# Optimization experiments

Measured on AMD Instinct MI355X. Metric: run time of the kernel, lower is better.

## Reference

```python
import jax, jax.numpy as jnp
import numpy as np

DIM = 1024
HEADS = 16
DIM_HEAD = 64
INNER = HEADS * DIM_HEAD  # 1024
MLP = 4096
EPS = 1e-5


def layer_norm(x, gamma, beta):
    mu = jnp.mean(x, axis=-1, keepdims=True)
    var = jnp.var(x, axis=-1, keepdims=True)
    return (x - mu) * jax.lax.rsqrt(var + EPS) * gamma + beta


def setup_inputs() -> dict:
    key = jax.random.key(0)
    ks = jax.random.split(key, 10)
    s = 0.02
    return {
        "x": jax.random.normal(ks[0], (2, 2048, DIM), dtype=jnp.float32),
        "ln1_g": jnp.ones((DIM,), jnp.float32),
        "ln1_b": jnp.zeros((DIM,), jnp.float32),
        "w_qkv": jax.random.normal(ks[1], (DIM, 3 * INNER), jnp.float32) * s,
        "w_out": jax.random.normal(ks[2], (INNER, DIM), jnp.float32) * s,
        "b_out": jnp.zeros((DIM,), jnp.float32),
        "ln2_g": jnp.ones((DIM,), jnp.float32),
        "ln2_b": jnp.zeros((DIM,), jnp.float32),
        "w1": jax.random.normal(ks[3], (DIM, MLP), jnp.float32) * s,
        "b1": jnp.zeros((MLP,), jnp.float32),
        "w2": jax.random.normal(ks[4], (MLP, DIM), jnp.float32) * s,
        "b2": jnp.zeros((DIM,), jnp.float32),
    }


def reference(x, ln1_g, ln1_b, w_qkv, w_out, b_out, ln2_g, ln2_b, w1, b1, w2, b2):
    b, n, _ = x.shape
    scale = DIM_HEAD ** -0.5

    # --- attention sublayer (pre-norm) ---
    h = layer_norm(x, ln1_g, ln1_b)
    qkv = h @ w_qkv  # [b, n, 3*inner]
    q, k, v = jnp.split(qkv, 3, axis=-1)
    # [b, n, inner] -> [b, heads, n, dim_head]
    def to_heads(t):
        return t.reshape(b, n, HEADS, DIM_HEAD).transpose(0, 2, 1, 3)
    q, k, v = to_heads(q), to_heads(k), to_heads(v)
    dots = jnp.einsum('bhid,bhjd->bhij', q, k) * scale  # [b,h,n,n]
    attn = jax.nn.softmax(dots, axis=-1)
    out = jnp.einsum('bhij,bhjd->bhid', attn, v)
    out = out.transpose(0, 2, 1, 3).reshape(b, n, INNER)
    x = out @ w_out + b_out + x

    # --- FFN sublayer (pre-norm) ---
    h = layer_norm(x, ln2_g, ln2_b)
    h = jax.nn.gelu(h @ w1 + b1, approximate=False)
    x = h @ w2 + b2 + x
    return x
```

## Files before the change

### kernel.cpp

```cpp
#include <hip/hip_runtime.h>
#include <hip/hip_bf16.h>
#include <math.h>

#define SEQ 2048
#define BATCH 2
#define TOKENS 4096
#define HEADS 16
#define DHEAD 64
#define TOKSTRIDE 3072

typedef __attribute__((ext_vector_type(4))) float f32x4;
typedef __attribute__((ext_vector_type(16))) float f32x16;
typedef __attribute__((ext_vector_type(8))) __bf16 bf16x8;
typedef __attribute__((ext_vector_type(8))) unsigned short ushort8;
typedef __attribute__((ext_vector_type(4))) unsigned short ushort4_t;
typedef __attribute__((ext_vector_type(4))) unsigned u32x4;
typedef __attribute__((ext_vector_type(2))) unsigned u32x2;

#if __has_builtin(__builtin_amdgcn_exp2f)
#define EXP2(x) __builtin_amdgcn_exp2f(x)
#else
#define EXP2(x) exp2f(x)
#endif

#if __has_builtin(__builtin_amdgcn_permlane32_swap)
#define HAS_PL32 1
#else
#define HAS_PL32 0
#endif

__device__ __forceinline__ unsigned short f2bf(float f) {
  unsigned u = __builtin_bit_cast(unsigned, f);
  u += 0x7fffu + ((u >> 16) & 1u);
  return (unsigned short)(u >> 16);
}

__device__ __forceinline__ float bf2f(unsigned short s) {
  unsigned u = ((unsigned)s) << 16;
  return __builtin_bit_cast(float, u);
}

__device__ __forceinline__ unsigned cvt_pk_bf16(float lo, float hi) {
  unsigned r;
  asm("v_cvt_pk_bf16_f32 %0, %1, %2" : "=v"(r) : "v"(lo), "v"(hi));
  return r;
}

__device__ __forceinline__ void cp16(const void* g, void* l) {
  __builtin_amdgcn_global_load_lds((const __attribute__((address_space(1))) void*)g,
                                   (__attribute__((address_space(3))) void*)l, 16, 0, 0);
}

#define FENCE asm volatile("" ::: "memory")
#define BARR  do { FENCE; __builtin_amdgcn_s_barrier(); FENCE; } while (0)

__global__ __launch_bounds__(256) void ln_rows(const float* __restrict__ x,
                                               const float* __restrict__ g,
                                               const float* __restrict__ b,
                                               unsigned short* __restrict__ out) {
  const int row = blockIdx.x;
  const int t = threadIdx.x;
  const f32x4* x4 = (const f32x4*)(x + (size_t)row * 1024);
  f32x4 v = x4[t];
  float sum = v[0] + v[1] + v[2] + v[3];
  float ss  = v[0]*v[0] + v[1]*v[1] + v[2]*v[2] + v[3]*v[3];
#pragma unroll
  for (int off = 1; off < 64; off <<= 1) {
    sum += __shfl_xor(sum, off);
    ss  += __shfl_xor(ss, off);
  }
  __shared__ float red[8];
  const int w = t >> 6, l = t & 63;
  if (l == 0) { red[w] = sum; red[w + 4] = ss; }
  __syncthreads();
  sum = red[0] + red[1] + red[2] + red[3];
  ss  = red[4] + red[5] + red[6] + red[7];
  const float mean = sum * (1.0f / 1024.0f);
  const float var  = ss * (1.0f / 1024.0f) - mean * mean;
  const float rs = rsqrtf(var + 1e-5f);
  ushort4_t o;
#pragma unroll
  for (int j = 0; j < 4; ++j) {
    float gv = g[t * 4 + j], bv = b[t * 4 + j];
    o[j] = f2bf((v[j] - mean) * rs * gv + bv);
  }
  *(ushort4_t*)(out + (size_t)row * 1024 + t * 4) = o;
}

__global__ __launch_bounds__(256) void ln_rows_bf(const unsigned short* __restrict__ x,
                                                  const float* __restrict__ g,
                                                  const float* __restrict__ b,
                                                  unsigned short* __restrict__ out) {
  const int row = blockIdx.x;
  const int t = threadIdx.x;
  ushort4_t v4 = *(const ushort4_t*)(x + (size_t)row * 1024 + t * 4);
  float v[4] = {bf2f(v4[0]), bf2f(v4[1]), bf2f(v4[2]), bf2f(v4[3])};
  float sum = v[0] + v[1] + v[2] + v[3];
  float ss  = v[0]*v[0] + v[1]*v[1] + v[2]*v[2] + v[3]*v[3];
#pragma unroll
  for (int off = 1; off < 64; off <<= 1) {
    sum += __shfl_xor(sum, off);
    ss  += __shfl_xor(ss, off);
  }
  __shared__ float red[8];
  const int w = t >> 6, l = t & 63;
  if (l == 0) { red[w] = sum; red[w + 4] = ss; }
  __syncthreads();
  sum = red[0] + red[1] + red[2] + red[3];
  ss  = red[4] + red[5] + red[6] + red[7];
  const float mean = sum * (1.0f / 1024.0f);
  const float var  = ss * (1.0f / 1024.0f) - mean * mean;
  const float rs = rsqrtf(var + 1e-5f);
  ushort4_t o;
#pragma unroll
  for (int j = 0; j < 4; ++j) {
    float gv = g[t * 4 + j], bv = b[t * 4 + j];
    o[j] = f2bf((v[j] - mean) * rs * gv + bv);
  }
  *(ushort4_t*)(out + (size_t)row * 1024 + t * 4) = o;
}

__global__ __launch_bounds__(256) void transpose_cast(const float* __restrict__ w,
                                                      unsigned short* __restrict__ wt,
                                                      int K, int N, float scale, int nscaled) {
  __shared__ float tile[32][33];
  const int n0 = blockIdx.x * 32, k0 = blockIdx.y * 32;
  const int tx = threadIdx.x & 31;
  const int ty = threadIdx.x >> 5;
#pragma unroll
  for (int i = 0; i < 4; ++i)
    tile[ty + 8 * i][tx] = w[(size_t)(k0 + ty + 8 * i) * N + n0 + tx];
  __syncthreads();
#pragma unroll
  for (int i = 0; i < 4; ++i) {
    int n = n0 + ty + 8 * i;
    float s = (n < nscaled) ? scale : 1.0f;
    wt[(size_t)n * K + k0 + tx] = f2bf(tile[tx][ty + 8 * i] * s);
  }
}

template <int EPI, int BN, int MINW>
__global__ __launch_bounds__(256, MINW) void gemm_bt(
    const unsigned short* __restrict__ A, const unsigned short* __restrict__ Bt,
    void* __restrict__ Cp, const float* __restrict__ bias, const void* __restrict__ resv,
    int M, int N, int K) {
  constexpr int BM = 128, BK = 64;
  constexpr int MR = BM / 32, NR = BN / 32;
  constexpr int AIT = BM * BK / 2048;
  constexpr int BIT = BN * BK / 2048;
  __shared__ unsigned short la[BM * BK];
  __shared__ unsigned short lb[BN * BK];
  const int t = threadIdx.x;
  const int w = t >> 6, l = t & 63;
  const int nwg = gridDim.x;
  const int bid = blockIdx.x;
  const int bid2 = (bid & 7) * (nwg >> 3) + (bid >> 3);
  const int nx = N / BN;
  const int m0 = (bid2 / nx) * BM, n0 = (bid2 % nx) * BN;
  const int wr = w >> 1, wc = w & 1;
  const int lrow = l & 15, lk4 = l >> 4;
  f32x4 acc[MR][NR] = {};

  for (int k0 = 0; k0 < K; k0 += BK) {
#pragma unroll
    for (int i = 0; i < AIT; ++i) {
      int idx = t + 256 * i;
      int row = idx >> 3, seg = idx & 7;
      int ss = seg ^ (row & 7);
      cp16(A + (size_t)(m0 + row) * K + k0 + ss * 8, (char*)la + w * 1024 + i * 4096);
    }
#pragma unroll
    for (int i = 0; i < BIT; ++i) {
      int idx = t + 256 * i;
      int row = idx >> 3, seg = idx & 7;
      int ss = seg ^ (row & 7);
      cp16(Bt + (size_t)(n0 + row) * K + k0 + ss * 8, (char*)lb + w * 1024 + i * 4096);
    }
    __syncthreads();
#pragma unroll
    for (int ks = 0; ks < 2; ++ks) {
      bf16x8 af[MR], bfr[NR];
#pragma unroll
      for (int mi = 0; mi < MR; ++mi) {
        int row = wr * (BM / 2) + mi * 16 + lrow;
        int ss = (ks * 4 + lk4) ^ (row & 7);
        af[mi] = *(const bf16x8*)((const char*)la + row * 128 + ss * 16);
      }
#pragma unroll
      for (int ni = 0; ni < NR; ++ni) {
        int row = wc * (BN / 2) + ni * 16 + lrow;
        int ss = (ks * 4 + lk4) ^ (row & 7);
        bfr[ni] = *(const bf16x8*)((const char*)lb + row * 128 + ss * 16);
      }
#pragma unroll
      for (int mi = 0; mi < MR; ++mi)
#pragma unroll
        for (int ni = 0; ni < NR; ++ni)
          acc[mi][ni] = __builtin_amdgcn_mfma_f32_16x16x32_bf16(af[mi], bfr[ni], acc[mi][ni], 0, 0, 0);
    }
    __syncthreads();
  }

#pragma unroll
  for (int mi = 0; mi < MR; ++mi) {
    int rowb = m0 + wr * (BM / 2) + mi * 16 + lk4 * 4;
#pragma unroll
    for (int ni = 0; ni < NR; ++ni) {
      int col = n0 + wc * (BN / 2) + ni * 16 + lrow;
      f32x4 a = acc[mi][ni];
#pragma unroll
      for (int r = 0; r < 4; ++r) {
        size_t off = (size_t)(rowb + r) * N + col;
        if (EPI == 0) {
          ((unsigned short*)Cp)[off] = f2bf(a[r]);
        } else if (EPI == 2) {
          float v = a[r] + bias[col];
          ((unsigned short*)Cp)[off] = f2bf(0.5f * v * (1.0f + erff(v * 0.70710678f)));
        } else if (EPI == 3) {
          ((unsigned short*)Cp)[off] = f2bf(a[r] + bias[col] + ((const float*)resv)[off]);
        } else {
          ((float*)Cp)[off] = a[r] + bias[col] + bf2f(((const unsigned short*)resv)[off]);
        }
      }
    }
  }
}

__global__ __launch_bounds__(256, 2) void attn4(const unsigned short* __restrict__ qkv,
                                                unsigned short* __restrict__ Op,
                                                float2* __restrict__ ml) {
  __shared__ unsigned short lk_[64 * 64];
  __shared__ unsigned short lvt[64 * 64];
  const int t = threadIdx.x, wv = t >> 6, l = t & 63;
  const int chunk = blockIdx.x & 3, qb = blockIdx.x >> 2;
  const int h = blockIdx.y, b = blockIdx.z;
  const size_t tok0 = (size_t)b * SEQ;
  const int lq = l & 31, hi = l >> 5, l7 = l & 7;
  const int qrow = qb * 128 + wv * 32 + lq;
  const int kstart = chunk * 8;

  bf16x8 qf[4];
#pragma unroll
  for (int dc = 0; dc < 4; ++dc)
    qf[dc] = *(const bf16x8*)(qkv + (tok0 + qrow) * TOKSTRIDE + h * DHEAD + dc * 16 + hi * 8);

  float mrun = -1e30f, lsum = 0.0f;
  f32x16 o0 = {}, o1 = {};

  {
#pragma unroll
    for (int i = 0; i < 2; ++i) {
      int idx = t + 256 * i;
      int key = idx >> 3, seg = idx & 7;
      cp16(qkv + (tok0 + kstart * 64 + key) * TOKSTRIDE + 1024 + h * DHEAD + ((seg ^ (key & 7)) << 3),
           (char*)lk_ + wv * 1024 + i * 4096);
    }
#pragma unroll
    for (int i = 0; i < 2; ++i) {
      int idx = t + 256 * i;
      int key = idx & 63, seg = idx >> 6;
      ushort8 v8 = *(const ushort8*)(qkv + (tok0 + kstart * 64 + key) * TOKSTRIDE + 2048 + h * DHEAD + seg * 8);
#pragma unroll
      for (int j = 0; j < 8; ++j) {
        int d = seg * 8 + j;
        lvt[d * 64 + (((key >> 3) ^ (d & 7)) << 3) + (key & 7)] = v8[j];
      }
    }
  }
  __syncthreads();

  for (int kb = 0; kb < 8; ++kb) {
    const bool more = (kb + 1 < 8);
    const int kpre = kstart + kb + 1;

    f32x16 s0 = {}, s1 = {};
    __builtin_amdgcn_s_setprio(1);
#pragma unroll
    for (int dc = 0; dc < 4; ++dc) {
      int sgA = (dc * 2 + hi) ^ l7;
      bf16x8 kf0 = *(const bf16x8*)((const char*)lk_ + lq * 128 + (sgA << 4));
      bf16x8 kf1 = *(const bf16x8*)((const char*)lk_ + (32 + lq) * 128 + (sgA << 4));
      s0 = __builtin_amdgcn_mfma_f32_32x32x16_bf16(kf0, qf[dc], s0, 0, 0, 0);
      s1 = __builtin_amdgcn_mfma_f32_32x32x16_bf16(kf1, qf[dc], s1, 0, 0, 0);
    }
    __builtin_amdgcn_s_setprio(0);

    asm volatile("s_waitcnt lgkmcnt(0)" ::: "memory");
    BARR;
    __builtin_amdgcn_sched_barrier(0);

    ushort8 vpre[2];
    if (more) {
#pragma unroll
      for (int i = 0; i < 2; ++i) {
        int idx = t + 256 * i;
        int key = idx >> 3, seg = idx & 7;
        cp16(qkv + (tok0 + kpre * 64 + key) * TOKSTRIDE + 1024 + h * DHEAD + ((seg ^ (key & 7)) << 3),
             (char*)lk_ + wv * 1024 + i * 4096);
      }
#pragma unroll
      for (int i = 0; i < 2; ++i) {
        int idx = t + 256 * i;
        int key = idx & 63, seg = idx >> 6;
        vpre[i] = *(const ushort8*)(qkv + (tok0 + kpre * 64 + key) * TOKSTRIDE + 2048 + h * DHEAD + seg * 8);
      }
    }

    float mx[8];
#pragma unroll
    for (int r = 0; r < 8; ++r)
      mx[r] = fmaxf(fmaxf(s0[r], s0[r + 8]), fmaxf(s1[r], s1[r + 8]));
#pragma unroll
    for (int r = 0; r < 4; ++r) mx[r] = fmaxf(mx[r], mx[r + 4]);
    float m01 = fmaxf(fmaxf(mx[0], mx[1]), fmaxf(mx[2], mx[3]));
    float pm = fmaxf(m01, __shfl_xor(m01, 32));

    if (__any(pm > mrun + 8.0f)) {
      float mn = fmaxf(mrun, pm);
      float alpha = EXP2(mrun - mn);
      mrun = mn;
      lsum *= alpha;
#pragma unroll
      for (int r = 0; r < 16; ++r) {
        int qi = (r & 3) + 8 * (r >> 2) + 4 * hi;
        float ar = __shfl(alpha, qi);
        o0[r] *= ar; o1[r] *= ar;
      }
    }

    float p0[16], p1[16], ts[16];
#pragma unroll
    for (int r = 0; r < 16; ++r) { p0[r] = EXP2(s0[r] - mrun); }
#pragma unroll
    for (int r = 0; r < 16; ++r) { p1[r] = EXP2(s1[r] - mrun); }
#pragma unroll
    for (int r = 0; r < 16; ++r) ts[r] = p0[r] + p1[r];
#pragma unroll
    for (int st = 8; st > 0; st >>= 1)
#pragma unroll
      for (int r = 0; r < 8; ++r)
        if (r < st) ts[r] += ts[r + st];
    float psum = ts[0] + __shfl_xor(ts[0], 32);
    lsum += psum;

    unsigned W0[8], W1[8];
#pragma unroll
    for (int mI = 0; mI < 8; ++mI) {
      W0[mI] = cvt_pk_bf16(p0[2 * mI], p0[2 * mI + 1]);
      W1[mI] = cvt_pk_bf16(p1[2 * mI], p1[2 * mI + 1]);
    }
#if !HAS_PL32
    unsigned X0[8], X1[8];
#pragma unroll
    for (int mI = 0; mI < 8; ++mI) {
      X0[mI] = __shfl_xor((int)W0[mI], 32);
      X1[mI] = __shfl_xor((int)W1[mI], 32);
    }
#endif

    __builtin_amdgcn_s_setprio(1);
#pragma unroll
    for (int kt = 0; kt < 2; ++kt) {
#pragma unroll
      for (int c = 0; c < 2; ++c) {
        u32x4 fw;
#if HAS_PL32
        unsigned a0 = (kt == 0) ? W0[4 * c + 0] : W1[4 * c + 0];
        unsigned a1 = (kt == 0) ? W0[4 * c + 1] : W1[4 * c + 1];
        unsigned b0 = (kt == 0) ? W0[4 * c + 2] : W1[4 * c + 2];
        unsigned b1 = (kt == 0) ? W0[4 * c + 3] : W1[4 * c + 3];
        u32x2 pa = __builtin_amdgcn_permlane32_swap(a0, b0, false, false);
        u32x2 pb = __builtin_amdgcn_permlane32_swap(a1, b1, false, false);
        fw[0] = pa[0]; fw[1] = pb[0]; fw[2] = pa[1]; fw[3] = pb[1];
#else
        if (kt == 0) {
          fw[0] = hi ? X0[4 * c + 2] : W0[4 * c + 0];
          fw[1] = hi ? X0[4 * c + 3] : W0[4 * c + 1];
          fw[2] = hi ? W0[4 * c + 2] : X0[4 * c + 0];
          fw[3] = hi ? W0[4 * c + 3] : X0[4 * c + 1];
        } else {
          fw[0] = hi ? X1[4 * c + 2] : W1[4 * c + 0];
          fw[1] = hi ? X1[4 * c + 3] : W1[4 * c + 1];
          fw[2] = hi ? W1[4 * c + 2] : X1[4 * c + 0];
          fw[3] = hi ? W1[4 * c + 3] : X1[4 * c + 1];
        }
#endif
        bf16x8 pf = __builtin_bit_cast(bf16x8, fw);
        int ksg = (kt * 4 + c * 2 + hi) ^ l7;
        bf16x8 vfA = *(const bf16x8*)((const char*)lvt + lq * 128 + (ksg << 4));
        bf16x8 vfB = *(const bf16x8*)((const char*)lvt + (32 + lq) * 128 + (ksg << 4));
        o0 = __builtin_amdgcn_mfma_f32_32x32x16_bf16(pf, vfA, o0, 0, 0, 0);
        o1 = __builtin_amdgcn_mfma_f32_32x32x16_bf16(pf, vfB, o1, 0, 0, 0);
      }
    }
    __builtin_amdgcn_s_setprio(0);

    asm volatile("s_waitcnt lgkmcnt(0)" ::: "memory");
    BARR;
    __builtin_amdgcn_sched_barrier(0);

    if (more) {
#pragma unroll
      for (int i = 0; i < 2; ++i) {
        int idx = t + 256 * i;
        int key = idx & 63, seg = idx >> 6;
#pragma unroll
        for (int j = 0; j < 8; ++j) {
          int d = seg * 8 + j;
          lvt[d * 64 + (((key >> 3) ^ (d & 7)) << 3) + (key & 7)] = vpre[i][j];
        }
      }
    }
    asm volatile("s_waitcnt vmcnt(0) lgkmcnt(0)" ::: "memory");
    BARR;
    __builtin_amdgcn_sched_barrier(0);
  }

  const size_t cbase = (size_t)chunk * TOKENS;
#pragma unroll
  for (int r = 0; r < 16; ++r) {
    int qi = (r & 3) + 8 * (r >> 2) + 4 * hi;
    size_t rowoff = (cbase + tok0 + qb * 128 + wv * 32 + qi) * (size_t)1024 + h * DHEAD;
    Op[rowoff + lq]      = f2bf(o0[r]);
    Op[rowoff + 32 + lq] = f2bf(o1[r]);
  }
  if (l < 32) {
    size_t tokr = tok0 + qb * 128 + wv * 32 + lq;
    ml[(cbase + tokr) * 16 + h] = make_float2(mrun, lsum);
  }
}

__global__ __launch_bounds__(256) void attn_combine4(const unsigned short* __restrict__ Op,
                                                     const float2* __restrict__ ml,
                                                     unsigned short* __restrict__ out) {
  const int t = threadIdx.x, w = t >> 6, l = t & 63;
  const size_t tok = blockIdx.x * 4 + w;
#pragma unroll
  for (int h = 0; h < 16; ++h) {
    float2 mm[4];
#pragma unroll
    for (int c = 0; c < 4; ++c) mm[c] = ml[((size_t)c * TOKENS + tok) * 16 + h];
    float M = fmaxf(fmaxf(mm[0].x, mm[1].x), fmaxf(mm[2].x, mm[3].x));
    float wgt[4];
    float den = 0.0f;
#pragma unroll
    for (int c = 0; c < 4; ++c) { wgt[c] = EXP2(mm[c].x - M); den += mm[c].y * wgt[c]; }
    float inv = 1.0f / den;
    int col = h * 64 + l;
    float o = 0.0f;
#pragma unroll
    for (int c = 0; c < 4; ++c)
      o += bf2f(Op[((size_t)c * TOKENS + tok) * 1024 + col]) * wgt[c];
    out[tok * 1024 + col] = f2bf(o * inv);
  }
}

extern "C" void kernel_launch(void* const* d_in, const int* in_sizes, int n_in,
                              void* d_out, int out_size, void* d_ws, size_t ws_size,
                              hipStream_t stream) {
  const float* x    = (const float*)d_in[0];
  const float* ln1g = (const float*)d_in[1];
  const float* ln1b = (const float*)d_in[2];
  const float* wqkv = (const float*)d_in[3];
  const float* wout = (const float*)d_in[4];
  const float* bout = (const float*)d_in[5];
  const float* ln2g = (const float*)d_in[6];
  const float* ln2b = (const float*)d_in[7];
  const float* w1   = (const float*)d_in[8];
  const float* b1   = (const float*)d_in[9];
  const float* w2   = (const float*)d_in[10];
  const float* b2   = (const float*)d_in[11];

  char* ws = (char*)d_ws;
  unsigned short* wqkvT = (unsigned short*)ws; ws += (size_t)3072 * 1024 * 2;
  unsigned short* woutT = (unsigned short*)ws; ws += (size_t)1024 * 1024 * 2;
  unsigned short* w1T   = (unsigned short*)ws; ws += (size_t)4096 * 1024 * 2;
  unsigned short* w2T   = (unsigned short*)ws; ws += (size_t)1024 * 4096 * 2;
  unsigned short* h1    = (unsigned short*)ws; ws += (size_t)TOKENS * 1024 * 2;
  unsigned short* qkvb  = (unsigned short*)ws; ws += (size_t)TOKENS * 3072 * 2;
  unsigned short* attno = (unsigned short*)ws; ws += (size_t)TOKENS * 1024 * 2;
  unsigned short* xa    = (unsigned short*)ws; ws += (size_t)TOKENS * 1024 * 4;
  unsigned short* h2    = (unsigned short*)ws; ws += (size_t)TOKENS * 1024 * 2;
  unsigned short* hid   = (unsigned short*)ws; ws += (size_t)TOKENS * 4096 * 2;
  float2*         mlbuf = (float2*)ws;         ws += (size_t)4 * TOKENS * 16 * 8;
  unsigned short* Opart = hid;

  transpose_cast<<<dim3(3072 / 32, 1024 / 32), 256, 0, stream>>>(wqkv, wqkvT, 1024, 3072, 0.18033688f, 1024);
  transpose_cast<<<dim3(1024 / 32, 1024 / 32), 256, 0, stream>>>(wout, woutT, 1024, 1024, 1.0f, 0);
  transpose_cast<<<dim3(4096 / 32, 1024 / 32), 256, 0, stream>>>(w1, w1T, 1024, 4096, 1.0f, 0);
  transpose_cast<<<dim3(1024 / 32, 4096 / 32), 256, 0, stream>>>(w2, w2T, 4096, 1024, 1.0f, 0);

  ln_rows<<<TOKENS, 256, 0, stream>>>(x, ln1g, ln1b, h1);
  gemm_bt<0, 128, 2><<<768, 256, 0, stream>>>(h1, wqkvT, qkvb, nullptr, nullptr, TOKENS, 3072, 1024);
  attn4<<<dim3(4 * SEQ / 128, HEADS, BATCH), 256, 0, stream>>>(qkvb, Opart, mlbuf);
  attn_combine4<<<TOKENS / 4, 256, 0, stream>>>(Opart, mlbuf, attno);
  gemm_bt<3, 64, 3><<<512, 256, 0, stream>>>(attno, woutT, xa, bout, x, TOKENS, 1024, 1024);
  ln_rows_bf<<<TOKENS, 256, 0, stream>>>(xa, ln2g, ln2b, h2);
  gemm_bt<2, 128, 2><<<1024, 256, 0, stream>>>(h2, w1T, hid, b1, nullptr, TOKENS, 4096, 1024);
  gemm_bt<4, 64, 3><<<512, 256, 0, stream>>>(hid, w2T, (float*)d_out, b2, xa, TOKENS, 1024, 4096);
}
```

Baseline: 247.4 us.

## Split-K the second MLP GEMM with wider tiles and a separate combine kernel

```diff
diff --git a/kernel.cpp b/kernel.cpp
--- a/kernel.cpp
+++ b/kernel.cpp
@@ -139,7 +139,7 @@
   }
 }
 
-template <int EPI, int BN, int MINW>
+template <int EPI, int BN, int MINW, int NSPLIT>
 __global__ __launch_bounds__(256, MINW) void gemm_bt(
     const unsigned short* __restrict__ A, const unsigned short* __restrict__ Bt,
     void* __restrict__ Cp, const float* __restrict__ bias, const void* __restrict__ resv,
@@ -155,13 +155,18 @@
   const int nwg = gridDim.x;
   const int bid = blockIdx.x;
   const int bid2 = (bid & 7) * (nwg >> 3) + (bid >> 3);
+  const int nmn = nwg / NSPLIT;
+  const int ksl = bid2 / nmn;
+  const int rmn = bid2 - ksl * nmn;
   const int nx = N / BN;
-  const int m0 = (bid2 / nx) * BM, n0 = (bid2 % nx) * BN;
+  const int m0 = (rmn / nx) * BM, n0 = (rmn % nx) * BN;
+  const int klen = K / NSPLIT;
+  const int kbeg = ksl * klen;
   const int wr = w >> 1, wc = w & 1;
   const int lrow = l & 15, lk4 = l >> 4;
   f32x4 acc[MR][NR] = {};
 
-  for (int k0 = 0; k0 < K; k0 += BK) {
+  for (int k0 = kbeg; k0 < kbeg + klen; k0 += BK) {
 #pragma unroll
     for (int i = 0; i < AIT; ++i) {
       int idx = t + 256 * i;
@@ -218,12 +223,30 @@
           ((unsigned short*)Cp)[off] = f2bf(0.5f * v * (1.0f + erff(v * 0.70710678f)));
         } else if (EPI == 3) {
           ((unsigned short*)Cp)[off] = f2bf(a[r] + bias[col] + ((const float*)resv)[off]);
+        } else if (EPI == 4) {
+          ((float*)Cp)[off] = a[r] + bias[col] + bf2f(((const unsigned short*)resv)[off]);
         } else {
-          ((float*)Cp)[off] = a[r] + bias[col] + bf2f(((const unsigned short*)resv)[off]);
+          ((float*)Cp)[(size_t)ksl * M * N + off] = a[r];
         }
       }
     }
   }
+}
+
+__global__ __launch_bounds__(256) void mlp2_combine(const float* __restrict__ p,
+                                                    const float* __restrict__ b2,
+                                                    const unsigned short* __restrict__ xa,
+                                                    float* __restrict__ out) {
+  const int row = blockIdx.x, t = threadIdx.x;
+  const size_t off = (size_t)row * 1024 + t * 4;
+  f32x4 a = *(const f32x4*)(p + off);
+  f32x4 b = *(const f32x4*)(p + (size_t)TOKENS * 1024 + off);
+  f32x4 bb = *(const f32x4*)(b2 + t * 4);
+  ushort4_t xv = *(const ushort4_t*)(xa + off);
+  f32x4 o;
+#pragma unroll
+  for (int j = 0; j < 4; ++j) o[j] = a[j] + b[j] + bb[j] + bf2f(xv[j]);
+  *(f32x4*)(out + off) = o;
 }
 
 __global__ __launch_bounds__(256, 2) void attn4(const unsigned short* __restrict__ qkv,
@@ -484,6 +507,7 @@
   unsigned short* hid   = (unsigned short*)ws; ws += (size_t)TOKENS * 4096 * 2;
   float2*         mlbuf = (float2*)ws;         ws += (size_t)4 * TOKENS * 16 * 8;
   unsigned short* Opart = hid;
+  float*          mlp2p = (float*)h1;
 
   transpose_cast<<<dim3(3072 / 32, 1024 / 32), 256, 0, stream>>>(wqkv, wqkvT, 1024, 3072, 0.18033688f, 1024);
   transpose_cast<<<dim3(1024 / 32, 1024 / 32), 256, 0, stream>>>(wout, woutT, 1024, 1024, 1.0f, 0);
@@ -491,11 +515,12 @@
   transpose_cast<<<dim3(1024 / 32, 4096 / 32), 256, 0, stream>>>(w2, w2T, 4096, 1024, 1.0f, 0);
 
   ln_rows<<<TOKENS, 256, 0, stream>>>(x, ln1g, ln1b, h1);
-  gemm_bt<0, 128, 2><<<768, 256, 0, stream>>>(h1, wqkvT, qkvb, nullptr, nullptr, TOKENS, 3072, 1024);
+  gemm_bt<0, 128, 2, 1><<<768, 256, 0, stream>>>(h1, wqkvT, qkvb, nullptr, nullptr, TOKENS, 3072, 1024);
   attn4<<<dim3(4 * SEQ / 128, HEADS, BATCH), 256, 0, stream>>>(qkvb, Opart, mlbuf);
   attn_combine4<<<TOKENS / 4, 256, 0, stream>>>(Opart, mlbuf, attno);
-  gemm_bt<3, 64, 3><<<512, 256, 0, stream>>>(attno, woutT, xa, bout, x, TOKENS, 1024, 1024);
+  gemm_bt<3, 64, 3, 1><<<512, 256, 0, stream>>>(attno, woutT, xa, bout, x, TOKENS, 1024, 1024);
   ln_rows_bf<<<TOKENS, 256, 0, stream>>>(xa, ln2g, ln2b, h2);
-  gemm_bt<2, 128, 2><<<1024, 256, 0, stream>>>(h2, w1T, hid, b1, nullptr, TOKENS, 4096, 1024);
-  gemm_bt<4, 64, 3><<<512, 256, 0, stream>>>(hid, w2T, (float*)d_out, b2, xa, TOKENS, 1024, 4096);
-}
+  gemm_bt<2, 128, 2, 1><<<1024, 256, 0, stream>>>(h2, w1T, hid, b1, nullptr, TOKENS, 4096, 1024);
+  gemm_bt<5, 128, 2, 2><<<512, 256, 0, stream>>>(hid, w2T, mlp2p, nullptr, nullptr, TOKENS, 1024, 4096);
+  mlp2_combine<<<TOKENS, 256, 0, stream>>>(mlp2p, b2, xa, (float*)d_out);
+}
```

Result: no change. 242.6 us (-1.9%).
